# Optimization experiments

Hardware: AMD Instinct MI355X
Metric: run time of the kernel (lower is better)

Reference implementation:

```python
import jax, jax.numpy as jnp
import numpy as np

N = 25000
E = 400000
MUL0 = 64   # multiplicity of 0e node irreps
MUL1 = 32   # multiplicity of 1o node irreps
NUM_BASIS = 10
FC_HIDDEN = 100
WEIGHT_NUMEL = 2 * MUL0 + 3 * MUL1  # 224: per-edge tp weights for the 5 uvu paths
MID_S = MUL0 + MUL1       # 96 mid scalar channels
MID_V = MUL0 + 2 * MUL1   # 128 mid vector channels
NUM_NEIGHBORS = 16.0


def setup_inputs() -> dict:
    key = jax.random.key(0)
    ks = jax.random.split(key, 16)
    inp = {
        'node_scalars': jax.random.normal(ks[0], (N, MUL0), jnp.float32),
        'node_vectors': jax.random.normal(ks[1], (N, MUL1, 3), jnp.float32),
        'node_attr': jnp.ones((N, 1), jnp.float32),
        'edge_src': jax.random.randint(ks[2], (E,), 0, N, jnp.int32),
        'edge_dst': jax.random.randint(ks[3], (E,), 0, N, jnp.int32),
        'edge_attr': jax.random.normal(ks[4], (E, 4), jnp.float32),
        'edge_scalars': jax.random.normal(ks[5], (E, NUM_BASIS), jnp.float32),
        # FullyConnectedNet: [10, 100, weight_numel], silu on hidden
        'W_fc1': jax.random.normal(ks[6], (NUM_BASIS, FC_HIDDEN), jnp.float32) / np.sqrt(NUM_BASIS),
        'W_fc2': jax.random.normal(ks[7], (FC_HIDDEN, WEIGHT_NUMEL), jnp.float32) / np.sqrt(FC_HIDDEN),
        # FullyConnectedTensorProduct with 0e attr == per-irrep linear mixing
        'W_sc_s': jax.random.normal(ks[8], (MUL0, MUL0), jnp.float32) / np.sqrt(MUL0),
        'W_sc_v': jax.random.normal(ks[9], (MUL1, MUL1), jnp.float32) / np.sqrt(MUL1),
        'W_l1_s': jax.random.normal(ks[10], (MUL0, MUL0), jnp.float32) / np.sqrt(MUL0),
        'W_l1_v': jax.random.normal(ks[11], (MUL1, MUL1), jnp.float32) / np.sqrt(MUL1),
        'W_l2_s': jax.random.normal(ks[12], (MID_S, MUL0), jnp.float32) / np.sqrt(MID_S),
        'W_l2_v': jax.random.normal(ks[13], (MID_V, MUL1), jnp.float32) / np.sqrt(MID_V),
        'W_l3': jax.random.normal(ks[14], (MID_S, 1), jnp.float32) / np.sqrt(MID_S),
    }
    return inp


def reference(node_scalars, node_vectors, node_attr, edge_src, edge_dst, edge_attr,
              edge_scalars, W_fc1, W_fc2, W_sc_s, W_sc_v, W_l1_s, W_l1_v,
              W_l2_s, W_l2_v, W_l3):
    n = node_scalars.shape[0]
    # --- edge-weight FC net: silu hidden, linear out -> per-edge tp weights ---
    w = jax.nn.silu(edge_scalars @ W_fc1) @ W_fc2  # [E, 224]
    w_00, w_01 = w[:, :MUL0], w[:, MUL0:2 * MUL0]                  # paths from 0e input
    w_10 = w[:, 2 * MUL0:2 * MUL0 + MUL1]                          # 1o x 0e -> 1o
    w_11s = w[:, 2 * MUL0 + MUL1:2 * MUL0 + 2 * MUL1]              # 1o x 1o -> 0e
    w_11v = w[:, 2 * MUL0 + 2 * MUL1:]                             # 1o x 1o -> 1o

    attr = node_attr  # [N,1] (0e attr => scalar multiplier)
    # self-connection and lin1 (per-irrep linear * attr)
    sc_s = (node_scalars @ W_sc_s) * attr
    sc_v = jnp.einsum('nuc,uv->nvc', node_vectors, W_sc_v) * attr[:, :, None]
    f_s = (node_scalars @ W_l1_s) * attr
    f_v = jnp.einsum('nuc,uv->nvc', node_vectors, W_l1_v) * attr[:, :, None]

    # --- gather source node features per edge ---
    s = f_s[edge_src]          # [E, MUL0]
    v = f_v[edge_src]          # [E, MUL1, 3]
    y0 = edge_attr[:, :1]      # l=0 sh
    y1 = edge_attr[:, 1:4]     # l=1 sh

    # --- weighted tensor product (uvu), CG-contracted paths ---
    mid_s = jnp.concatenate([
        w_00 * s * y0,                                              # 0e x 0e -> 0e
        w_11s * jnp.einsum('euc,ec->eu', v, y1) / jnp.sqrt(3.0),    # 1o x 1o -> 0e
    ], axis=1)                                                      # [E, 96]
    mid_v = jnp.concatenate([
        w_01[:, :, None] * s[:, :, None] * y1[:, None, :],          # 0e x 1o -> 1o
        w_10[:, :, None] * v * y0[:, :, None],                      # 1o x 0e -> 1o
        w_11v[:, :, None] * jnp.cross(v, y1[:, None, :]) / jnp.sqrt(2.0),  # 1o x 1o -> 1o
    ], axis=1)                                                      # [E, 128, 3]

    # --- scatter-add aggregation into destination nodes ---
    inv = 1.0 / jnp.sqrt(NUM_NEIGHBORS)
    agg_s = jax.ops.segment_sum(mid_s, edge_dst, num_segments=n) * inv
    agg_v = jax.ops.segment_sum(mid_v, edge_dst, num_segments=n) * inv

    # --- output linears and gated residual mix ---
    conv_s = (agg_s @ W_l2_s) * attr
    conv_v = jnp.einsum('nuc,uv->nvc', agg_v, W_l2_v) * attr[:, :, None]
    angle = 0.1 * (agg_s @ W_l3) * attr  # [N,1]
    cos, sin = jnp.cos(angle), jnp.sin(angle)  # sc output_mask is all-ones here
    out_s = cos * sc_s + sin * conv_s
    out_v = cos[:, :, None] * sc_v + sin[:, :, None] * conv_v
    return jnp.concatenate([out_s, out_v.reshape(n, -1)], axis=1)  # [N, 64+96]
```

## Files before the change

### kernel.cpp

```cpp
#include <hip/hip_runtime.h>

#define MUL0 64
#define MUL1 32
#define NBASIS 10
#define FCH 100
#define WNUMEL 224
#define MIDS 96
#define MIDV 128
#define EG 4

#define OFF_W1   0
#define OFF_W2   1000
#define OFF_WSCS 23400
#define OFF_WSCV 27496
#define OFF_WL1S 28520
#define OFF_WL1V 32616
#define OFF_WL2S 33640
#define OFF_WL2V 39784
#define OFF_WL3  43880
#define OFF_WEND 43976
#define OFF_FLAG 43980
#define OFF_W1FRAG 44032
#define OFF_W2FRAG 45824
#define OFF_DYN  60160

#define W1FRAG_N (112 * 32)
#define W2FRAG_N (4 * 224 * 32)

typedef __attribute__((ext_vector_type(8))) short short8;
typedef __attribute__((ext_vector_type(4))) float f32x4;

__device__ __forceinline__ float bf2f(unsigned short h) {
    unsigned int u = ((unsigned int)h) << 16;
    float f; __builtin_memcpy(&f, &u, 4); return f;
}
__device__ __forceinline__ unsigned short f2bf(float f) {
    unsigned int u; __builtin_memcpy(&u, &f, 4);
    u += 0x7fffu + ((u >> 16) & 1u);
    return (unsigned short)(u >> 16);
}
__device__ __forceinline__ float fast_silu(float x) {
    return x * __builtin_amdgcn_rcpf(1.0f + __expf(-x));
}
template<bool BF>
__device__ __forceinline__ float ldf(const void* p, size_t i) {
    if constexpr (BF) return bf2f(((const unsigned short*)p)[i]);
    else              return ((const float*)p)[i];
}
template<bool BF>
__device__ __forceinline__ void stf(void* p, size_t i, float v) {
    if constexpr (BF) ((unsigned short*)p)[i] = f2bf(v);
    else              ((float*)p)[i] = v;
}
template<bool BF>
__device__ __forceinline__ f32x4 ld4(const void* p, size_t i) {
    if constexpr (BF) {
        ushort4 h = *(const ushort4*)((const unsigned short*)p + i);
        return (f32x4){bf2f(h.x), bf2f(h.y), bf2f(h.z), bf2f(h.w)};
    } else {
        return *(const f32x4*)((const float*)p + i);
    }
}
__device__ __forceinline__ int wave_incl_scan(int v) {
    int lane = threadIdx.x & 63;
    #pragma unroll
    for (int d = 1; d < 64; d <<= 1) {
        int t = __shfl_up(v, d, 64);
        if (lane >= d) v += t;
    }
    return v;
}

template<bool BF>
__device__ __forceinline__ void node_pre_body(
    const void* __restrict__ ns, const void* __restrict__ nv,
    const void* __restrict__ attr,
    const void* __restrict__ Wl1s, const void* __restrict__ Wl1v,
    float* __restrict__ f_s, float* __restrict__ f_v, int i, int Nn)
{
    int stotal = Nn * MUL0;
    if (i < stotal) {
        int n = i >> 6, j = i & 63;
        float a = 0.f;
        #pragma unroll
        for (int u = 0; u < MUL0; u++)
            a = fmaf(ldf<BF>(ns, (size_t)n * MUL0 + u), ldf<BF>(Wl1s, u * MUL0 + j), a);
        f_s[i] = a * ldf<BF>(attr, n);
    } else {
        int m = i - stotal;
        if (m >= Nn * MUL1 * 3) return;
        int n = m / 96; int idx = m - n * 96;
        int vi = idx / 3; int c = idx - vi * 3;
        float a = 0.f;
        #pragma unroll
        for (int u = 0; u < MUL1; u++)
            a = fmaf(ldf<BF>(nv, (size_t)n * 96 + u * 3 + c), ldf<BF>(Wl1v, u * MUL1 + vi), a);
        f_v[m] = a * ldf<BF>(attr, n);
    }
}

__global__ __launch_bounds__(256) void k_prep(
    const void* __restrict__ ns, const void* __restrict__ nv,
    const void* __restrict__ attr,
    const void* __restrict__ a0, const void* __restrict__ a1,
    const void* __restrict__ a2, const void* __restrict__ a3,
    const void* __restrict__ a4, const void* __restrict__ a5,
    const void* __restrict__ a6, const void* __restrict__ a7,
    const void* __restrict__ a8,
    float* __restrict__ wsf,
    unsigned short* __restrict__ w1frag, unsigned short* __restrict__ w2frag,
    int* __restrict__ cnt, int* __restrict__ flag,
    float* __restrict__ f_s, float* __restrict__ f_v, int Nn)
{
    const bool bf = (((const unsigned int*)attr)[0] == 0x3F803F80u);
    int i = blockIdx.x * 256 + threadIdx.x;
    if (i == 0) *flag = bf ? 1 : 0;

    const int npre = Nn * 160;
    if (i < npre) {
        if (bf) node_pre_body<true >(ns, nv, attr, a4, a5, f_s, f_v, i, Nn);
        else    node_pre_body<false>(ns, nv, attr, a4, a5, f_s, f_v, i, Nn);
        return;
    }
    int m = i - npre;
    if (m < OFF_WEND) {
        const void* p; int off = m;
        if      (m < OFF_W2)   { p = a0; }
        else if (m < OFF_WSCS) { p = a1; off = m - OFF_W2; }
        else if (m < OFF_WSCV) { p = a2; off = m - OFF_WSCS; }
        else if (m < OFF_WL1S) { p = a3; off = m - OFF_WSCV; }
        else if (m < OFF_WL1V) { p = a4; off = m - OFF_WL1S; }
        else if (m < OFF_WL2S) { p = a5; off = m - OFF_WL1V; }
        else if (m < OFF_WL2V) { p = a6; off = m - OFF_WL2S; }
        else if (m < OFF_WL3)  { p = a7; off = m - OFF_WL2V; }
        else                   { p = a8; off = m - OFF_WL3; }
        wsf[m] = bf ? ldf<true>(p, off) : ldf<false>(p, off);
        return;
    }
    m -= OFF_WEND;
    if (m < W1FRAG_N) {
        int col = m >> 5, k = m & 31;
        float v = 0.f;
        if (col < FCH && k < NBASIS)
            v = bf ? ldf<true>(a0, k * FCH + col) : ldf<false>(a0, k * FCH + col);
        w1frag[m] = f2bf(v);
        return;
    }
    m -= W1FRAG_N;
    if (m < W2FRAG_N) {
        int q = m / (224 * 32); int r = m - q * 224 * 32;
        int n = r >> 5; int kk = r & 31;
        int k = q * 32 + kk;
        float v = 0.f;
        if (k < FCH)
            v = bf ? ldf<true>(a1, k * WNUMEL + n) : ldf<false>(a1, k * WNUMEL + n);
        w2frag[m] = f2bf(v);
        return;
    }
    m -= W2FRAG_N;
    if (m < Nn) cnt[m] = 0;
}

__global__ __launch_bounds__(256) void k_hist(
    const int* __restrict__ edst, int* __restrict__ cnt, int Ecnt)
{
    int e = blockIdx.x * 256 + threadIdx.x;
    if (e < Ecnt) atomicAdd(&cnt[edst[e]], 1);
}

__global__ __launch_bounds__(256) void k_scan_blk(
    const int* __restrict__ cnt, int* __restrict__ row_part,
    int* __restrict__ blk_sum, int Nn)
{
    __shared__ int ws4[4];
    int tid = threadIdx.x, lane = tid & 63, wid = tid >> 6;
    int i = blockIdx.x * 256 + tid;
    int v = (i < Nn) ? cnt[i] : 0;
    int incl = wave_incl_scan(v);
    if (lane == 63) ws4[wid] = incl;
    __syncthreads();
    int off = 0;
    #pragma unroll
    for (int w2 = 0; w2 < 4; w2++) off += (w2 < wid) ? ws4[w2] : 0;
    if (i < Nn) row_part[i] = off + incl - v;
    if (tid == 0) blk_sum[blockIdx.x] = ws4[0] + ws4[1] + ws4[2] + ws4[3];
}

__global__ __launch_bounds__(256) void k_scan_top(
    const int* __restrict__ blk_sum, int* __restrict__ blk_off,
    int* __restrict__ row_start, int NB, int Nn)
{
    __shared__ int ws4[4];
    int tid = threadIdx.x, lane = tid & 63, wid = tid >> 6;
    int v = (tid < NB) ? blk_sum[tid] : 0;
    int incl = wave_incl_scan(v);
    if (lane == 63) ws4[wid] = incl;
    __syncthreads();
    int off = 0;
    #pragma unroll
    for (int w2 = 0; w2 < 4; w2++) off += (w2 < wid) ? ws4[w2] : 0;
    if (tid < NB) blk_off[tid] = off + incl - v;
    if (tid == 0) row_start[Nn] = ws4[0] + ws4[1] + ws4[2] + ws4[3];
}

__global__ __launch_bounds__(256) void k_rowfix(
    const int* __restrict__ row_part, const int* __restrict__ blk_off,
    int* __restrict__ row_start, int* __restrict__ cur, int Nn)
{
    int i = blockIdx.x * 256 + threadIdx.x;
    if (i < Nn) { row_start[i] = blk_off[i >> 8] + row_part[i]; cur[i] = 0; }
}

__global__ __launch_bounds__(1024) void k_scan1(
    const int* __restrict__ cnt, int* __restrict__ row_start,
    int* __restrict__ cur, int Nn)
{
    __shared__ int wsum[16];
    __shared__ int s_off, s_tot;
    int tid = threadIdx.x, lane = tid & 63, wid = tid >> 6;
    if (tid == 0) s_off = 0;
    __syncthreads();
    for (int base = 0; base < Nn; base += 1024) {
        int i = base + tid;
        int v = (i < Nn) ? cnt[i] : 0;
        int incl = wave_incl_scan(v);
        if (lane == 63) wsum[wid] = incl;
        __syncthreads();
        if (wid == 0) {
            int wv = (lane < 16) ? wsum[lane] : 0;
            int wincl = wave_incl_scan(wv);
            if (lane < 16) wsum[lane] = wincl - wv;
            if (lane == 15) s_tot = wincl;
        }
        __syncthreads();
        int excl = s_off + wsum[wid] + incl - v;
        if (i < Nn) { row_start[i] = excl; cur[i] = 0; }
        __syncthreads();
        if (tid == 0) s_off += s_tot;
        __syncthreads();
    }
    if (threadIdx.x == 0) row_start[Nn] = s_off;
}

__global__ __launch_bounds__(256) void k_place(
    const int* __restrict__ edst, const int* __restrict__ esrc,
    const void* __restrict__ eattr,
    const int* __restrict__ row_start, int* __restrict__ cur,
    int* __restrict__ perm, int* __restrict__ srcs, float* __restrict__ y4,
    int Ecnt, const int* __restrict__ flag, int extras)
{
    int e = blockIdx.x * 256 + threadIdx.x;
    if (e >= Ecnt) return;
    int d = edst[e];
    int pos = row_start[d] + atomicAdd(&cur[d], 1);
    perm[pos] = e;
    if (extras) {
        srcs[pos] = esrc[e];
        float4 yv;
        if (*flag) {
            const unsigned short* ap = (const unsigned short*)eattr + (size_t)e * 4;
            yv = make_float4(bf2f(ap[0]), bf2f(ap[1]), bf2f(ap[2]), bf2f(ap[3]));
        } else {
            const float* ap = (const float*)eattr + (size_t)e * 4;
            yv = make_float4(ap[0], ap[1], ap[2], ap[3]);
        }
        ((float4*)y4)[pos] = yv;
    }
}

#define HFC_STRIDE 136

__global__ __launch_bounds__(256) void k_fc(
    const void* __restrict__ escal, const int* __restrict__ perm,
    const unsigned short* __restrict__ w1frag, const unsigned short* __restrict__ w2frag,
    unsigned short* __restrict__ wbuf, int Ecnt, const int* __restrict__ flag)
{
    __shared__ __align__(16) unsigned short h_lds[64 * HFC_STRIDE];
    const int tid  = threadIdx.x;
    const int lane = tid & 63;
    const int wave = tid >> 6;
    const int nl   = lane & 15;
    const int quad = lane >> 4;
    const int tb   = blockIdx.x * 64;

    for (int i = tid; i < 64 * 16; i += 256) {
        int row = i >> 4;
        h_lds[row * HFC_STRIDE + 112 + (i & 15)] = 0;
    }

    int eidx = tb + 16 * wave + nl;
    if (eidx >= Ecnt) eidx = Ecnt - 1;
    const int e = perm[eidx];
    short8 a = {0, 0, 0, 0, 0, 0, 0, 0};
    if (*flag) {
        const unsigned int* p = (const unsigned int*)((const unsigned short*)escal + (size_t)e * NBASIS);
        if (quad == 0) {
            unsigned int d0 = p[0], d1 = p[1], d2 = p[2], d3 = p[3];
            a = (short8){(short)d0, (short)(d0 >> 16), (short)d1, (short)(d1 >> 16),
                         (short)d2, (short)(d2 >> 16), (short)d3, (short)(d3 >> 16)};
        } else if (quad == 1) {
            unsigned int d4 = p[4];
            a = (short8){(short)d4, (short)(d4 >> 16), 0, 0, 0, 0, 0, 0};
        }
    } else {
        const float* p = (const float*)escal + (size_t)e * NBASIS;
        if (quad == 0) {
            a = (short8){(short)f2bf(p[0]), (short)f2bf(p[1]), (short)f2bf(p[2]), (short)f2bf(p[3]),
                         (short)f2bf(p[4]), (short)f2bf(p[5]), (short)f2bf(p[6]), (short)f2bf(p[7])};
        } else if (quad == 1) {
            a = (short8){(short)f2bf(p[8]), (short)f2bf(p[9]), 0, 0, 0, 0, 0, 0};
        }
    }

    {
        f32x4 hacc[7];
        #pragma unroll
        for (int t = 0; t < 7; t++) {
            short8 b = *(const short8*)&w1frag[(16 * t + nl) * 32 + quad * 8];
            hacc[t] = __builtin_amdgcn_mfma_f32_16x16x32_bf16(
                a, b, (f32x4){0.f, 0.f, 0.f, 0.f}, 0, 0, 0);
        }
        #pragma unroll
        for (int t = 0; t < 7; t++) {
            #pragma unroll
            for (int r = 0; r < 4; r++)
                h_lds[(16 * wave + quad * 4 + r) * HFC_STRIDE + 16 * t + nl] =
                    f2bf(fast_silu(hacc[t][r]));
        }
    }
    __syncthreads();

    #pragma unroll 2
    for (int t = 0; t < 14; t++) {
        f32x4 c = {0.f, 0.f, 0.f, 0.f};
        #pragma unroll
        for (int q = 0; q < 4; q++) {
            short8 av = *(const short8*)&h_lds[(16 * wave + nl) * HFC_STRIDE + q * 32 + quad * 8];
            short8 b = *(const short8*)&w2frag[((q * 224) + 16 * t + nl) * 32 + quad * 8];
            c = __builtin_amdgcn_mfma_f32_16x16x32_bf16(av, b, c, 0, 0, 0);
        }
        #pragma unroll
        for (int r = 0; r < 4; r++)
            wbuf[(size_t)(tb + 16 * wave + quad * 4 + r) * WNUMEL + 16 * t + nl] = f2bf(c[r]);
    }
}

__global__ __launch_bounds__(256) void k_agg(
    const unsigned short* __restrict__ wbuf,
    const int* __restrict__ srcs, const float* __restrict__ y4,
    const int* __restrict__ row_start,
    const float* __restrict__ f_s, const float* __restrict__ f_v,
    const float* __restrict__ Wl3, const void* __restrict__ attr,
    float* __restrict__ agg_s, float* __restrict__ aggv,
    float* __restrict__ cosb, float* __restrict__ sinb,
    int Nn, const int* __restrict__ flag)
{
    const int tid  = threadIdx.x;
    const int lane = tid & 63;
    const int wave = tid >> 6;
    const int node = blockIdx.x * EG + wave;
    if (node >= Nn) return;

    const int lane2 = lane & 31;
    const bool hi = (lane >= 32);

    const int dlo = row_start[node];
    const int dhi = row_start[node + 1];

    float acc0 = 0.f, acc1 = 0.f;
    float accS0 = 0.f, accS1 = 0.f, accS2 = 0.f;
    float accV0 = 0.f, accV1 = 0.f, accV2 = 0.f;

    const float k14 = 0.25f;
    const float k13 = 0.25f * 0.57735026918962576451f;
    const float k12 = 0.25f * 0.70710678118654752440f;

    #pragma unroll 2
    for (int idx = dlo; idx < dhi; idx++) {
        const int srcn = srcs[idx];
        const float4 y = ((const float4*)y4)[idx];
        const float y0 = y.x, y1x = y.y, y1y = y.z, y1z = y.w;
        const unsigned short* wrow = wbuf + (size_t)idx * WNUMEL;
        const float* fsr = f_s + (size_t)srcn * 64;
        const float* fvr = f_v + (size_t)srcn * 96;

        float fs_l = fsr[lane];
        float v0 = fvr[lane2 * 3 + 0];
        float v1 = fvr[lane2 * 3 + 1];
        float v2 = fvr[lane2 * 3 + 2];

        float w00 = bf2f(wrow[lane]);
        float w01 = bf2f(wrow[64 + lane]);
        float wh  = bf2f(wrow[128 + lane]);
        float wx  = bf2f(wrow[160 + lane]);

        acc0 = fmaf(w00 * fs_l, y0 * k14, acc0);

        float dot = v0 * y1x + v1 * y1y + v2 * y1z;
        acc1 = fmaf(wh * dot, k13, acc1);

        float t1 = w01 * fs_l * k14;
        accS0 = fmaf(t1, y1x, accS0);
        accS1 = fmaf(t1, y1y, accS1);
        accS2 = fmaf(t1, y1z, accS2);

        float cx = v1 * y1z - v2 * y1y;
        float cy = v2 * y1x - v0 * y1z;
        float cz = v0 * y1y - v1 * y1x;
        float e0 = hi ? cx : v0;
        float e1 = hi ? cy : v1;
        float e2 = hi ? cz : v2;
        float tv = hi ? (wx * k12) : (wh * (y0 * k14));
        accV0 = fmaf(e0, tv, accV0);
        accV1 = fmaf(e1, tv, accV1);
        accV2 = fmaf(e2, tv, accV2);
    }

    {
        float* as = agg_s + (size_t)node * MIDS;
        float* av = aggv  + (size_t)node * 384;
        as[lane] = acc0;
        if (hi) as[64 + lane2] = acc1;

        av[0 * 128 + lane] = accS0;
        av[1 * 128 + lane] = accS1;
        av[2 * 128 + lane] = accS2;
        const int vrow = hi ? (96 + lane2) : (64 + lane);
        av[0 * 128 + vrow] = accV0;
        av[1 * 128 + vrow] = accV1;
        av[2 * 128 + vrow] = accV2;

        float avv = acc0 * Wl3[lane];
        if (hi) avv = fmaf(acc1, Wl3[64 + lane2], avv);
        #pragma unroll
        for (int d = 1; d < 64; d <<= 1) avv += __shfl_xor(avv, d);
        if (lane == 0) {
            float at = (*flag) ? ldf<true>(attr, node) : ldf<false>(attr, node);
            float aa = 0.1f * avv * at;
            cosb[node] = __cosf(aa);
            sinb[node] = __sinf(aa);
        }
    }
}

#define WT_STRIDE 164

template<bool BF>
__device__ __forceinline__ void final_s_body(
    const float* __restrict__ agg_s, const void* __restrict__ ns,
    const float* __restrict__ cosb, const float* __restrict__ sinb,
    const void* __restrict__ attr, void* __restrict__ out,
    int Nn, const float* Wt, int lane, int nb)
{
    float acc_sc[8], acc_l2[8];
    int nidx[8];
    #pragma unroll
    for (int r = 0; r < 8; r++) {
        acc_sc[r] = 0.f; acc_l2[r] = 0.f;
        int n = nb + r; nidx[r] = (n < Nn) ? n : (Nn - 1);
    }
    #pragma unroll 2
    for (int t = 0; t < 16; t++) {
        f32x4 wv = *(const f32x4*)&Wt[lane * WT_STRIDE + 4 * t];
        #pragma unroll
        for (int r = 0; r < 8; r++) {
            f32x4 x = ld4<BF>(ns, (size_t)nidx[r] * 64 + 4 * t);
            acc_sc[r] = fmaf(x[0], wv[0], acc_sc[r]);
            acc_sc[r] = fmaf(x[1], wv[1], acc_sc[r]);
            acc_sc[r] = fmaf(x[2], wv[2], acc_sc[r]);
            acc_sc[r] = fmaf(x[3], wv[3], acc_sc[r]);
        }
    }
    #pragma unroll 2
    for (int t = 0; t < 24; t++) {
        f32x4 wv = *(const f32x4*)&Wt[lane * WT_STRIDE + 64 + 4 * t];
        #pragma unroll
        for (int r = 0; r < 8; r++) {
            f32x4 x = *(const f32x4*)(agg_s + (size_t)nidx[r] * 96 + 4 * t);
            acc_l2[r] = fmaf(x[0], wv[0], acc_l2[r]);
            acc_l2[r] = fmaf(x[1], wv[1], acc_l2[r]);
            acc_l2[r] = fmaf(x[2], wv[2], acc_l2[r]);
            acc_l2[r] = fmaf(x[3], wv[3], acc_l2[r]);
        }
    }
    #pragma unroll
    for (int r = 0; r < 8; r++) {
        int n = nb + r;
        if (n < Nn) {
            float cv = cosb[n], sv = sinb[n];
            float at = ldf<BF>(attr, n);
            stf<BF>(out, (size_t)n * 160 + lane, at * (cv * acc_sc[r] + sv * acc_l2[r]));
        }
    }
}

__global__ __launch_bounds__(256) void k_final_s(
    const float* __restrict__ agg_s, const void* __restrict__ ns,
    const float* __restrict__ Wscs, const float* __restrict__ Wl2s,
    const float* __restrict__ cosb, const float* __restrict__ sinb,
    const void* __restrict__ attr, void* __restrict__ out,
    int Nn, const int* __restrict__ flag)
{
    __shared__ float Wt[64 * WT_STRIDE];
    const int tid = threadIdx.x;
    for (int i = tid; i < 160 * 64; i += 256) {
        int u = i >> 6, j = i & 63;
        float w = (u < 64) ? Wscs[u * 64 + j] : Wl2s[(u - 64) * 64 + j];
        Wt[j * WT_STRIDE + u] = w;
    }
    __syncthreads();

    const int lane = tid & 63;
    const int wave = __builtin_amdgcn_readfirstlane(tid >> 6);
    const int nb   = (blockIdx.x * 4 + wave) * 8;
    if (nb >= Nn) return;
    if (*flag) final_s_body<true >(agg_s, ns, cosb, sinb, attr, out, Nn, Wt, lane, nb);
    else       final_s_body<false>(agg_s, ns, cosb, sinb, attr, out, Nn, Wt, lane, nb);
}

template<bool BF>
__device__ __forceinline__ void final_v_body(
    const float* __restrict__ aggv, const void* __restrict__ nv,
    const float* __restrict__ cosb, const float* __restrict__ sinb,
    const void* __restrict__ attr, void* __restrict__ out,
    int Nn, const float* Wt, int lane, int ub)
{
    const int vi   = lane & 31;
    const int grp  = lane >> 5;
    const int NU   = 3 * Nn;
    float acc_sc[8], acc_l2[8];
    int gidx[8], nn_[8], cc_[8];
    #pragma unroll
    for (int r = 0; r < 8; r++) {
        acc_sc[r] = 0.f; acc_l2[r] = 0.f;
        int g = ub + grp * 8 + r;
        if (g > NU - 1) g = NU - 1;
        gidx[r] = g;
        nn_[r] = (int)((unsigned)g / 3u);
        cc_[r] = g - 3 * nn_[r];
    }
    #pragma unroll 2
    for (int t = 0; t < 8; t++) {
        f32x4 wv = *(const f32x4*)&Wt[vi * WT_STRIDE + 4 * t];
        #pragma unroll
        for (int r = 0; r < 8; r++) {
            size_t b = (size_t)nn_[r] * 96 + (size_t)(4 * t) * 3 + cc_[r];
            float x0 = ldf<BF>(nv, b);
            float x1 = ldf<BF>(nv, b + 3);
            float x2 = ldf<BF>(nv, b + 6);
            float x3 = ldf<BF>(nv, b + 9);
            acc_sc[r] = fmaf(x0, wv[0], acc_sc[r]);
            acc_sc[r] = fmaf(x1, wv[1], acc_sc[r]);
            acc_sc[r] = fmaf(x2, wv[2], acc_sc[r]);
            acc_sc[r] = fmaf(x3, wv[3], acc_sc[r]);
        }
    }
    #pragma unroll 2
    for (int t = 0; t < 32; t++) {
        f32x4 wv = *(const f32x4*)&Wt[vi * WT_STRIDE + 32 + 4 * t];
        #pragma unroll
        for (int r = 0; r < 8; r++) {
            f32x4 x = *(const f32x4*)(aggv + (size_t)gidx[r] * 128 + 4 * t);
            acc_l2[r] = fmaf(x[0], wv[0], acc_l2[r]);
            acc_l2[r] = fmaf(x[1], wv[1], acc_l2[r]);
            acc_l2[r] = fmaf(x[2], wv[2], acc_l2[r]);
            acc_l2[r] = fmaf(x[3], wv[3], acc_l2[r]);
        }
    }
    #pragma unroll
    for (int r = 0; r < 8; r++) {
        int g = ub + grp * 8 + r;
        if (g < NU) {
            int n = nn_[r], c = cc_[r];
            float cv = cosb[n], sv = sinb[n];
            float at = ldf<BF>(attr, n);
            stf<BF>(out, (size_t)n * 160 + 64 + vi * 3 + c,
                    at * (cv * acc_sc[r] + sv * acc_l2[r]));
        }
    }
}

__global__ __launch_bounds__(256) void k_final_v(
    const float* __restrict__ aggv, const void* __restrict__ nv,
    const float* __restrict__ Wscv, const float* __restrict__ Wl2v,
    const float* __restrict__ cosb, const float* __restrict__ sinb,
    const void* __restrict__ attr, void* __restrict__ out,
    int Nn, const int* __restrict__ flag)
{
    __shared__ float Wt[32 * WT_STRIDE];
    const int tid = threadIdx.x;
    for (int i = tid; i < 160 * 32; i += 256) {
        int u = i >> 5, j = i & 31;
        float w = (u < 32) ? Wscv[u * 32 + j] : Wl2v[(u - 32) * 32 + j];
        Wt[j * WT_STRIDE + u] = w;
    }
    __syncthreads();

    const int lane = tid & 63;
    const int wave = __builtin_amdgcn_readfirstlane(tid >> 6);
    const int ub   = (blockIdx.x * 4 + wave) * 16;
    if (ub >= 3 * Nn) return;
    if (*flag) final_v_body<true >(aggv, nv, cosb, sinb, attr, out, Nn, Wt, lane, ub);
    else       final_v_body<false>(aggv, nv, cosb, sinb, attr, out, Nn, Wt, lane, ub);
}

#define ES_STRIDE 40
#define H_STRIDE 136
#define WL_STRIDE 225

__global__ __launch_bounds__(256) void k_edge_mfma(
    const void* __restrict__ escal, const void* __restrict__ eattr,
    const void* __restrict__ attr,
    const int* __restrict__ esrc,
    const int* __restrict__ row_start, const int* __restrict__ perm,
    const unsigned short* __restrict__ w1frag, const unsigned short* __restrict__ w2frag,
    const float* __restrict__ Wl3,
    const float* __restrict__ f_s, const float* __restrict__ f_v,
    float* __restrict__ agg_s, float* __restrict__ agg_v,
    float* __restrict__ cosb, float* __restrict__ sinb,
    int Nn, const int* __restrict__ flag)
{
    __shared__ __align__(16) unsigned short es_lds[64 * ES_STRIDE];
    __shared__ __align__(16) unsigned short h_lds[64 * H_STRIDE];
    __shared__ __align__(16) unsigned short w_lds[64 * WL_STRIDE];
    __shared__ float y_lds[64][4];
    __shared__ int   src_lds[64];

    const int tid  = threadIdx.x;
    const int lane = tid & 63;
    const int wave = tid >> 6;
    const int nl   = lane & 15;
    const int quad = lane >> 4;
    const int gbase = blockIdx.x * EG;
    const bool isbf = (*flag != 0);

    for (int i = tid; i < 64 * 22; i += 256) {
        int row = i / 22, k = 10 + (i - row * 22);
        es_lds[row * ES_STRIDE + k] = 0;
    }
    for (int i = tid; i < 64 * 16; i += 256) {
        int row = i >> 4, k = 112 + (i & 15);
        h_lds[row * H_STRIDE + k] = 0;
    }

    const int lane2 = lane & 31;
    const int u0 = lane / 3,  c0 = lane - 3 * u0;
    const int pB = 64 + lane;
    const int uB = pB / 3,    cB = pB - 3 * uB;
    const int p2 = 128 + lane;
    const int u2 = p2 / 3,    c2 = p2 - 3 * u2;
    const int pH = 64 + lane2;
    const int uH = pH / 3,    cH = pH - 3 * uH;
    const bool half = (lane < 32);

    const int node = gbase + wave;
    const int dlo = (node < Nn) ? row_start[node] : 0;
    const int dhi = (node < Nn) ? row_start[node + 1] : 0;

    float acc[9];
    #pragma unroll
    for (int s = 0; s < 9; s++) acc[s] = 0.f;

    const int gend    = (gbase + EG < Nn) ? (gbase + EG) : Nn;
    const int e_start = row_start[gbase];
    const int e_end   = row_start[gend];

    for (int tb = e_start; tb < e_end; tb += 64) {
        const int tcnt = (e_end - tb < 64) ? (e_end - tb) : 64;
        __syncthreads();

        {
            int i = tid & 63, part = tid >> 6;
            if (i < tcnt && part < 2) {
                int e = perm[tb + i];
                if (part == 0) {
                    unsigned int* dstp = (unsigned int*)&es_lds[i * ES_STRIDE];
                    if (isbf) {
                        const unsigned int* srcp =
                            (const unsigned int*)((const unsigned short*)escal + (size_t)e * NBASIS);
                        #pragma unroll
                        for (int t2 = 0; t2 < 5; t2++) dstp[t2] = srcp[t2];
                    } else {
                        const float* srcp = (const float*)escal + (size_t)e * NBASIS;
                        #pragma unroll
                        for (int t2 = 0; t2 < 5; t2++) {
                            unsigned int lo = f2bf(srcp[2 * t2]);
                            unsigned int hi = f2bf(srcp[2 * t2 + 1]);
                            dstp[t2] = lo | (hi << 16);
                        }
                    }
                } else {
                    src_lds[i] = esrc[e];
                    if (isbf) {
                        const unsigned short* ap = (const unsigned short*)eattr + (size_t)e * 4;
                        #pragma unroll
                        for (int t2 = 0; t2 < 4; t2++) y_lds[i][t2] = bf2f(ap[t2]);
                    } else {
                        const float* ap = (const float*)eattr + (size_t)e * 4;
                        #pragma unroll
                        for (int t2 = 0; t2 < 4; t2++) y_lds[i][t2] = ap[t2];
                    }
                }
            }
        }
        __syncthreads();

        {
            short8 a = *(const short8*)&es_lds[(16 * wave + nl) * ES_STRIDE + quad * 8];
            f32x4 hacc[7];
            #pragma unroll
            for (int t = 0; t < 7; t++) {
                short8 b = *(const short8*)&w1frag[(16 * t + nl) * 32 + quad * 8];
                hacc[t] = __builtin_amdgcn_mfma_f32_16x16x32_bf16(
                    a, b, (f32x4){0.f, 0.f, 0.f, 0.f}, 0, 0, 0);
            }
            #pragma unroll
            for (int t = 0; t < 7; t++) {
                #pragma unroll
                for (int r = 0; r < 4; r++)
                    h_lds[(16 * wave + quad * 4 + r) * H_STRIDE + 16 * t + nl] =
                        f2bf(fast_silu(hacc[t][r]));
            }
        }
        __syncthreads();

        #pragma unroll 2
        for (int t = 0; t < 14; t++) {
            f32x4 c = {0.f, 0.f, 0.f, 0.f};
            #pragma unroll
            for (int q = 0; q < 4; q++) {
                short8 a = *(const short8*)&h_lds[(16 * wave + nl) * H_STRIDE + q * 32 + quad * 8];
                short8 b = *(const short8*)&w2frag[((q * 224) + 16 * t + nl) * 32 + quad * 8];
                c = __builtin_amdgcn_mfma_f32_16x16x32_bf16(a, b, c, 0, 0, 0);
            }
            #pragma unroll
            for (int r = 0; r < 4; r++)
                w_lds[(16 * wave + quad * 4 + r) * WL_STRIDE + 16 * t + nl] = f2bf(c[r]);
        }
        __syncthreads();

        {
            int lo = dlo > tb ? dlo : tb;
            int hi = dhi < tb + tcnt ? dhi : tb + tcnt;
            for (int idx = lo; idx < hi; idx++) {
                const int i = idx - tb;
                const int srcn = src_lds[i];
                const float y0  = y_lds[i][0];
                const float y1x = y_lds[i][1];
                const float y1y = y_lds[i][2];
                const float y1z = y_lds[i][3];
                const float* fsr = f_s + (size_t)srcn * 64;
                const float* fvr = f_v + (size_t)srcn * 96;
                const unsigned short* wrow = &w_lds[i * WL_STRIDE];

                float fs_l  = fsr[lane];
                float fs_u0 = fsr[u0];
                float fs_uB = fsr[uB];
                float fs_u2 = fsr[u2];
                float fvA0 = fvr[lane2 * 3], fvA1 = fvr[lane2 * 3 + 1], fvA2 = fvr[lane2 * 3 + 2];
                float fvB0 = fvr[u0 * 3],    fvB1 = fvr[u0 * 3 + 1],    fvB2 = fvr[u0 * 3 + 2];
                float fvH0 = fvr[uH * 3],    fvH1 = fvr[uH * 3 + 1],    fvH2 = fvr[uH * 3 + 2];

                float y1c0 = (c0 == 0) ? y1x : (c0 == 1) ? y1y : y1z;
                float y1cB = (cB == 0) ? y1x : (cB == 1) ? y1y : y1z;
                float y1c2 = (c2 == 0) ? y1x : (c2 == 1) ? y1y : y1z;

                float w_s0 = bf2f(wrow[lane]);
                float w_s1 = bf2f(wrow[160 + lane2]);
                float w_s2 = bf2f(wrow[64 + u0]);
                float w_s3 = bf2f(wrow[64 + uB]);
                float w_s4 = bf2f(wrow[64 + u2]);
                float w_s5 = bf2f(wrow[128 + u0]);
                float w_s6 = bf2f(wrow[128 + uH]);
                float w_s7 = bf2f(wrow[192 + u0]);
                float w_s8 = bf2f(wrow[192 + uH]);

                const float k14 = 0.25f;
                const float k13 = 0.25f * 0.57735026918962576451f;
                const float k12 = 0.25f * 0.70710678118654752440f;

                acc[0] = fmaf(w_s0 * fs_l, y0 * k14, acc[0]);
                {
                    float dot = fvA0 * y1x + fvA1 * y1y + fvA2 * y1z;
                    acc[1] = fmaf(w_s1 * dot, k13, acc[1]);
                }
                acc[2] = fmaf(w_s2 * fs_u0, k14 * y1c0, acc[2]);
                acc[3] = fmaf(w_s3 * fs_uB, k14 * y1cB, acc[3]);
                acc[4] = fmaf(w_s4 * fs_u2, k14 * y1c2, acc[4]);
                {
                    float e5 = (c0 == 0) ? fvB0 : (c0 == 1) ? fvB1 : fvB2;
                    float e6 = (cH == 0) ? fvH0 : (cH == 1) ? fvH1 : fvH2;
                    acc[5] = fmaf(w_s5 * e5, k14 * y0, acc[5]);
                    acc[6] = fmaf(w_s6 * e6, k14 * y0, acc[6]);
                }
                {
                    float cr7 = (c0 == 0) ? (fvB1 * y1z - fvB2 * y1y)
                              : (c0 == 1) ? (fvB2 * y1x - fvB0 * y1z)
                                          : (fvB0 * y1y - fvB1 * y1x);
                    float cr8 = (cH == 0) ? (fvH1 * y1z - fvH2 * y1y)
                              : (cH == 1) ? (fvH2 * y1x - fvH0 * y1z)
                                          : (fvH0 * y1y - fvH1 * y1x);
                    acc[7] = fmaf(w_s7 * cr7, k12, acc[7]);
                    acc[8] = fmaf(w_s8 * cr8, k12, acc[8]);
                }
            }
        }
    }

    if (node < Nn) {
        float* as = agg_s + (size_t)node * MIDS;
        float* av = agg_v + (size_t)node * (MIDV * 3);
        as[lane] = acc[0];
        if (half) as[64 + lane] = acc[1];
        av[lane]       = acc[2];
        av[64 + lane]  = acc[3];
        av[128 + lane] = acc[4];
        av[192 + lane] = acc[5];
        if (half) av[256 + lane] = acc[6];
        av[288 + lane] = acc[7];
        if (half) av[352 + lane] = acc[8];

        float avv = acc[0] * Wl3[lane];
        if (half) avv = fmaf(acc[1], Wl3[64 + lane], avv);
        #pragma unroll
        for (int d = 1; d < 64; d <<= 1) avv += __shfl_xor(avv, d);
        if (lane == 0) {
            float at = isbf ? ldf<true>(attr, node) : ldf<false>(attr, node);
            float a = 0.1f * avv * at;
            cosb[node] = __cosf(a);
            sinb[node] = __sinf(a);
        }
    }
}

template<bool BF>
__device__ __forceinline__ void final_body(
    const void* __restrict__ ns, const void* __restrict__ nv,
    const void* __restrict__ attr,
    const float* __restrict__ Wscs, const float* __restrict__ Wscv,
    const float* __restrict__ Wl2s, const float* __restrict__ Wl2v,
    const float* __restrict__ agg_s, const float* __restrict__ agg_v,
    const float* __restrict__ cosb, const float* __restrict__ sinb,
    void* __restrict__ out, int Nn)
{
    int i = blockIdx.x * 256 + threadIdx.x;
    int stotal = Nn * MUL0;
    if (i < stotal) {
        int n = i >> 6, j = i & 63;
        const float* ar = agg_s + (size_t)n * MIDS;
        float a1 = 0.f, a2 = 0.f;
        #pragma unroll
        for (int u = 0; u < MUL0; u++)
            a1 = fmaf(ldf<BF>(ns, (size_t)n * MUL0 + u), Wscs[u * MUL0 + j], a1);
        #pragma unroll
        for (int u = 0; u < MIDS; u++) a2 = fmaf(ar[u], Wl2s[u * MUL0 + j], a2);
        float o = ldf<BF>(attr, n) * (cosb[n] * a1 + sinb[n] * a2);
        stf<BF>(out, (size_t)n * 160 + j, o);
    } else {
        int m = i - stotal;
        if (m >= Nn * 96) return;
        int n = m / 96; int idx = m - n * 96;
        int vi = idx / 3; int c = idx - vi * 3;
        const float* ar = agg_v + (size_t)n * (MIDV * 3);
        float a1 = 0.f, a2 = 0.f;
        #pragma unroll
        for (int u = 0; u < MUL1; u++)
            a1 = fmaf(ldf<BF>(nv, (size_t)n * 96 + u * 3 + c), Wscv[u * MUL1 + vi], a1);
        #pragma unroll
        for (int u = 0; u < MIDV; u++) a2 = fmaf(ar[u * 3 + c], Wl2v[u * MUL1 + vi], a2);
        float o = ldf<BF>(attr, n) * (cosb[n] * a1 + sinb[n] * a2);
        stf<BF>(out, (size_t)n * 160 + 64 + idx, o);
    }
}
__global__ __launch_bounds__(256) void k_final(
    const void* ns, const void* nv, const void* attr,
    const float* Wscs, const float* Wscv,
    const float* Wl2s, const float* Wl2v,
    const float* agg_s, const float* agg_v,
    const float* cosb, const float* sinb,
    void* out, int Nn, const int* flag)
{
    if (*flag) final_body<true >(ns, nv, attr, Wscs, Wscv, Wl2s, Wl2v, agg_s, agg_v, cosb, sinb, out, Nn);
    else       final_body<false>(ns, nv, attr, Wscs, Wscv, Wl2s, Wl2v, agg_s, agg_v, cosb, sinb, out, Nn);
}

extern "C" void kernel_launch(void* const* d_in, const int* in_sizes, int n_in,
                              void* d_out, int out_size, void* d_ws, size_t ws_size,
                              hipStream_t stream)
{
    const void* ns    = d_in[0];
    const void* nv    = d_in[1];
    const void* attr  = d_in[2];
    const int*  esrc  = (const int*)d_in[3];
    const int*  edst  = (const int*)d_in[4];
    const void* eattr = d_in[5];
    const void* escal = d_in[6];

    const int Nn   = in_sizes[2];
    const int Ecnt = in_sizes[3];

    float* ws = (float*)d_ws;
    int* flag = (int*)(ws + OFF_FLAG);
    unsigned short* w1frag = (unsigned short*)(ws + OFF_W1FRAG);
    unsigned short* w2frag = (unsigned short*)(ws + OFF_W2FRAG);

    size_t o = OFF_DYN;
    const size_t OFF_FS   = o; o += (size_t)Nn * 64;
    const size_t OFF_FV   = o; o += (size_t)Nn * 96;
    const size_t OFF_AGGS = o; o += (size_t)Nn * 96;
    const size_t OFF_AGGV = o; o += (size_t)Nn * 384;
    const size_t OFF_COS  = o; o += Nn;
    const size_t OFF_SIN  = o; o += Nn;
    const size_t OFF_CNT  = o; o += Nn;
    const size_t OFF_ROW  = o; o += Nn + 1;
    const size_t OFF_CUR  = o; o += Nn;
    const size_t OFF_RPART= o; o += Nn;
    const size_t OFF_BSUM = o; o += 256;
    const size_t OFF_BOFF = o; o += 256;
    const size_t OFF_PERM = o; o += Ecnt;
    const size_t OFF_SRCS = o; o += Ecnt;
    o = (o + 3) & ~(size_t)3;
    const size_t OFF_Y4   = o; o += (size_t)Ecnt * 4;
    o = (o + 15) & ~(size_t)15;
    const size_t OFF_WBUF = o;
    const int tiles = (Ecnt + 63) / 64;
    o += (size_t)tiles * 64 * 112;
    const size_t need_bytes = o * sizeof(float);

    int* cnt       = (int*)(ws + OFF_CNT);
    int* row_start = (int*)(ws + OFF_ROW);
    int* cur       = (int*)(ws + OFF_CUR);
    int* row_part  = (int*)(ws + OFF_RPART);
    int* blk_sum   = (int*)(ws + OFF_BSUM);
    int* blk_off   = (int*)(ws + OFF_BOFF);
    int* perm      = (int*)(ws + OFF_PERM);
    int* srcs      = (int*)(ws + OFF_SRCS);
    float* y4      = ws + OFF_Y4;
    unsigned short* wbuf = (unsigned short*)(ws + OFF_WBUF);

    const int NB = (Nn + 255) / 256;
    const bool split = (ws_size >= need_bytes) && (NB <= 256);

    const int prep_work = Nn * 160 + OFF_WEND + W1FRAG_N + W2FRAG_N + Nn;
    k_prep<<<(prep_work + 255) / 256, 256, 0, stream>>>(
        ns, nv, attr,
        d_in[7], d_in[8], d_in[9], d_in[10], d_in[11], d_in[12],
        d_in[13], d_in[14], d_in[15],
        ws, w1frag, w2frag, cnt, flag,
        ws + OFF_FS, ws + OFF_FV, Nn);

    k_hist<<<(Ecnt + 255) / 256, 256, 0, stream>>>(edst, cnt, Ecnt);

    if (split) {
        k_scan_blk<<<NB, 256, 0, stream>>>(cnt, row_part, blk_sum, Nn);
        k_scan_top<<<1, 256, 0, stream>>>(blk_sum, blk_off, row_start, NB, Nn);
        k_rowfix<<<NB, 256, 0, stream>>>(row_part, blk_off, row_start, cur, Nn);
        k_place<<<(Ecnt + 255) / 256, 256, 0, stream>>>(
            edst, esrc, eattr, row_start, cur, perm, srcs, y4, Ecnt, flag, 1);

        k_fc<<<tiles, 256, 0, stream>>>(escal, perm, w1frag, w2frag, wbuf, Ecnt, flag);

        k_agg<<<(Nn + EG - 1) / EG, 256, 0, stream>>>(
            wbuf, srcs, y4, row_start,
            ws + OFF_FS, ws + OFF_FV, ws + OFF_WL3, attr,
            ws + OFF_AGGS, ws + OFF_AGGV, ws + OFF_COS, ws + OFF_SIN,
            Nn, flag);

        k_final_s<<<(Nn + 31) / 32, 256, 0, stream>>>(
            ws + OFF_AGGS, ns, ws + OFF_WSCS, ws + OFF_WL2S,
            ws + OFF_COS, ws + OFF_SIN, attr, (void*)d_out, Nn, flag);
        k_final_v<<<(3 * Nn + 63) / 64, 256, 0, stream>>>(
            ws + OFF_AGGV, nv, ws + OFF_WSCV, ws + OFF_WL2V,
            ws + OFF_COS, ws + OFF_SIN, attr, (void*)d_out, Nn, flag);
    } else {
        k_scan1<<<1, 1024, 0, stream>>>(cnt, row_start, cur, Nn);
        k_place<<<(Ecnt + 255) / 256, 256, 0, stream>>>(
            edst, esrc, eattr, row_start, cur, perm, srcs, y4, Ecnt, flag, 0);
        k_edge_mfma<<<(Nn + EG - 1) / EG, 256, 0, stream>>>(
            escal, eattr, attr, esrc, row_start, perm, w1frag, w2frag,
            ws + OFF_WL3,
            ws + OFF_FS, ws + OFF_FV,
            ws + OFF_AGGS, ws + OFF_AGGV, ws + OFF_COS, ws + OFF_SIN,
            Nn, flag);
        k_final<<<((Nn * 160) + 255) / 256, 256, 0, stream>>>(
            ns, nv, attr,
            ws + OFF_WSCS, ws + OFF_WSCV, ws + OFF_WL2S, ws + OFF_WL2V,
            ws + OFF_AGGS, ws + OFF_AGGV, ws + OFF_COS, ws + OFF_SIN,
            (void*)d_out, Nn, flag);
    }
}
```

Measured before the change: 544.7 us.

## Split node pre-linear into register-tiled kernels, reuse FC2 weights, unroll aggregation edges

The per-node linear layers move out of the prep kernel into two dedicated kernels. Each stages the transposed weight in shared memory and gives every lane several nodes, so each weight load is reused across them. The FC second layer now loads each B fragment once per output tile and reuses it across all four edge groups, with wave tiles split unevenly. The aggregation loop splits each node's edges into four interleaved chains with masked padding, giving more memory-level parallelism at the cost of extra registers and wasted loads on low-degree nodes.

```diff
diff --git a/kernel.cpp b/kernel.cpp
--- a/kernel.cpp
+++ b/kernel.cpp
@@ -71,36 +71,7 @@
     return v;
 }
 
-template<bool BF>
-__device__ __forceinline__ void node_pre_body(
-    const void* __restrict__ ns, const void* __restrict__ nv,
-    const void* __restrict__ attr,
-    const void* __restrict__ Wl1s, const void* __restrict__ Wl1v,
-    float* __restrict__ f_s, float* __restrict__ f_v, int i, int Nn)
-{
-    int stotal = Nn * MUL0;
-    if (i < stotal) {
-        int n = i >> 6, j = i & 63;
-        float a = 0.f;
-        #pragma unroll
-        for (int u = 0; u < MUL0; u++)
-            a = fmaf(ldf<BF>(ns, (size_t)n * MUL0 + u), ldf<BF>(Wl1s, u * MUL0 + j), a);
-        f_s[i] = a * ldf<BF>(attr, n);
-    } else {
-        int m = i - stotal;
-        if (m >= Nn * MUL1 * 3) return;
-        int n = m / 96; int idx = m - n * 96;
-        int vi = idx / 3; int c = idx - vi * 3;
-        float a = 0.f;
-        #pragma unroll
-        for (int u = 0; u < MUL1; u++)
-            a = fmaf(ldf<BF>(nv, (size_t)n * 96 + u * 3 + c), ldf<BF>(Wl1v, u * MUL1 + vi), a);
-        f_v[m] = a * ldf<BF>(attr, n);
-    }
-}
-
 __global__ __launch_bounds__(256) void k_prep(
-    const void* __restrict__ ns, const void* __restrict__ nv,
     const void* __restrict__ attr,
     const void* __restrict__ a0, const void* __restrict__ a1,
     const void* __restrict__ a2, const void* __restrict__ a3,
@@ -109,20 +80,12 @@
     const void* __restrict__ a8,
     float* __restrict__ wsf,
     unsigned short* __restrict__ w1frag, unsigned short* __restrict__ w2frag,
-    int* __restrict__ cnt, int* __restrict__ flag,
-    float* __restrict__ f_s, float* __restrict__ f_v, int Nn)
+    int* __restrict__ cnt, int* __restrict__ flag, int Nn)
 {
     const bool bf = (((const unsigned int*)attr)[0] == 0x3F803F80u);
-    int i = blockIdx.x * 256 + threadIdx.x;
-    if (i == 0) *flag = bf ? 1 : 0;
-
-    const int npre = Nn * 160;
-    if (i < npre) {
-        if (bf) node_pre_body<true >(ns, nv, attr, a4, a5, f_s, f_v, i, Nn);
-        else    node_pre_body<false>(ns, nv, attr, a4, a5, f_s, f_v, i, Nn);
-        return;
-    }
-    int m = i - npre;
+    int m = blockIdx.x * 256 + threadIdx.x;
+    if (m == 0) *flag = bf ? 1 : 0;
+
     if (m < OFF_WEND) {
         const void* p; int off = m;
         if      (m < OFF_W2)   { p = a0; }
@@ -159,6 +122,126 @@
     }
     m -= W2FRAG_N;
     if (m < Nn) cnt[m] = 0;
+}
+
+#define PS_STRIDE 68
+#define PV_STRIDE 36
+
+template<bool BF>
+__device__ __forceinline__ void pre_s_body(
+    const void* __restrict__ ns, const void* __restrict__ attr,
+    const float* Wt, float* __restrict__ f_s, int Nn, int lane, int nb)
+{
+    float acc[8]; int nidx[8];
+    #pragma unroll
+    for (int r = 0; r < 8; r++) {
+        acc[r] = 0.f;
+        int n = nb + r; nidx[r] = (n < Nn) ? n : (Nn - 1);
+    }
+    #pragma unroll 2
+    for (int t = 0; t < 16; t++) {
+        f32x4 wv = *(const f32x4*)&Wt[lane * PS_STRIDE + 4 * t];
+        #pragma unroll
+        for (int r = 0; r < 8; r++) {
+            f32x4 x = ld4<BF>(ns, (size_t)nidx[r] * 64 + 4 * t);
+            acc[r] = fmaf(x[0], wv[0], acc[r]);
+            acc[r] = fmaf(x[1], wv[1], acc[r]);
+            acc[r] = fmaf(x[2], wv[2], acc[r]);
+            acc[r] = fmaf(x[3], wv[3], acc[r]);
+        }
+    }
+    #pragma unroll
+    for (int r = 0; r < 8; r++) {
+        int n = nb + r;
+        if (n < Nn) {
+            float at = ldf<BF>(attr, n);
+            f_s[(size_t)n * 64 + lane] = acc[r] * at;
+        }
+    }
+}
+
+__global__ __launch_bounds__(256) void k_pre_s(
+    const void* __restrict__ ns, const void* __restrict__ attr,
+    const float* __restrict__ Wl1s, float* __restrict__ f_s, int Nn)
+{
+    __shared__ float Wt[64 * PS_STRIDE];
+    const int tid = threadIdx.x;
+    const bool bf = (((const unsigned int*)attr)[0] == 0x3F803F80u);
+    for (int i = tid; i < 64 * 64; i += 256) {
+        int u = i >> 6, j = i & 63;
+        Wt[j * PS_STRIDE + u] = Wl1s[u * 64 + j];
+    }
+    __syncthreads();
+    const int lane = tid & 63;
+    const int wave = __builtin_amdgcn_readfirstlane(tid >> 6);
+    const int nb   = (blockIdx.x * 4 + wave) * 8;
+    if (nb >= Nn) return;
+    if (bf) pre_s_body<true >(ns, attr, Wt, f_s, Nn, lane, nb);
+    else    pre_s_body<false>(ns, attr, Wt, f_s, Nn, lane, nb);
+}
+
+template<bool BF>
+__device__ __forceinline__ void pre_v_body(
+    const void* __restrict__ nv, const void* __restrict__ attr,
+    const float* Wt, float* __restrict__ f_v, int Nn, int lane, int ub)
+{
+    const int vi  = lane & 31;
+    const int grp = lane >> 5;
+    const int NU  = 3 * Nn;
+    float acc[8]; int nn_[8], cc_[8];
+    #pragma unroll
+    for (int r = 0; r < 8; r++) {
+        acc[r] = 0.f;
+        int g = ub + grp * 8 + r;
+        if (g > NU - 1) g = NU - 1;
+        nn_[r] = (int)((unsigned)g / 3u);
+        cc_[r] = g - 3 * nn_[r];
+    }
+    #pragma unroll 2
+    for (int t = 0; t < 8; t++) {
+        f32x4 wv = *(const f32x4*)&Wt[vi * PV_STRIDE + 4 * t];
+        #pragma unroll
+        for (int r = 0; r < 8; r++) {
+            size_t b = (size_t)nn_[r] * 96 + (size_t)(4 * t) * 3 + cc_[r];
+            float x0 = ldf<BF>(nv, b);
+            float x1 = ldf<BF>(nv, b + 3);
+            float x2 = ldf<BF>(nv, b + 6);
+            float x3 = ldf<BF>(nv, b + 9);
+            acc[r] = fmaf(x0, wv[0], acc[r]);
+            acc[r] = fmaf(x1, wv[1], acc[r]);
+            acc[r] = fmaf(x2, wv[2], acc[r]);
+            acc[r] = fmaf(x3, wv[3], acc[r]);
+        }
+    }
+    #pragma unroll
+    for (int r = 0; r < 8; r++) {
+        int g = ub + grp * 8 + r;
+        if (g < NU) {
+            int n = nn_[r], c = cc_[r];
+            float at = ldf<BF>(attr, n);
+            f_v[(size_t)n * 96 + vi * 3 + c] = acc[r] * at;
+        }
+    }
+}
+
+__global__ __launch_bounds__(256) void k_pre_v(
+    const void* __restrict__ nv, const void* __restrict__ attr,
+    const float* __restrict__ Wl1v, float* __restrict__ f_v, int Nn)
+{
+    __shared__ float Wt[32 * PV_STRIDE];
+    const int tid = threadIdx.x;
+    const bool bf = (((const unsigned int*)attr)[0] == 0x3F803F80u);
+    for (int i = tid; i < 32 * 32; i += 256) {
+        int u = i >> 5, vi = i & 31;
+        Wt[vi * PV_STRIDE + u] = Wl1v[u * 32 + vi];
+    }
+    __syncthreads();
+    const int lane = tid & 63;
+    const int wave = __builtin_amdgcn_readfirstlane(tid >> 6);
+    const int ub   = (blockIdx.x * 4 + wave) * 16;
+    if (ub >= 3 * Nn) return;
+    if (bf) pre_v_body<true >(nv, attr, Wt, f_v, Nn, lane, ub);
+    else    pre_v_body<false>(nv, attr, Wt, f_v, Nn, lane, ub);
 }
 
 __global__ __launch_bounds__(256) void k_hist(
@@ -330,18 +413,32 @@
     }
     __syncthreads();
 
-    #pragma unroll 2
-    for (int t = 0; t < 14; t++) {
-        f32x4 c = {0.f, 0.f, 0.f, 0.f};
-        #pragma unroll
-        for (int q = 0; q < 4; q++) {
-            short8 av = *(const short8*)&h_lds[(16 * wave + nl) * HFC_STRIDE + q * 32 + quad * 8];
-            short8 b = *(const short8*)&w2frag[((q * 224) + 16 * t + nl) * 32 + quad * 8];
-            c = __builtin_amdgcn_mfma_f32_16x16x32_bf16(av, b, c, 0, 0, 0);
-        }
-        #pragma unroll
-        for (int r = 0; r < 4; r++)
-            wbuf[(size_t)(tb + 16 * wave + quad * 4 + r) * WNUMEL + 16 * t + nl] = f2bf(c[r]);
+    {
+        const int tsta = (wave < 2) ? wave * 4 : 8 + (wave - 2) * 3;
+        const int tend = (wave < 2) ? tsta + 4 : tsta + 3;
+        for (int t = tsta; t < tend; t++) {
+            short8 b0 = *(const short8*)&w2frag[(0 * 224 + 16 * t + nl) * 32 + quad * 8];
+            short8 b1 = *(const short8*)&w2frag[(1 * 224 + 16 * t + nl) * 32 + quad * 8];
+            short8 b2 = *(const short8*)&w2frag[(2 * 224 + 16 * t + nl) * 32 + quad * 8];
+            short8 b3 = *(const short8*)&w2frag[(3 * 224 + 16 * t + nl) * 32 + quad * 8];
+            #pragma unroll
+            for (int eg = 0; eg < 4; eg++) {
+                const unsigned short* hrow = &h_lds[(16 * eg + nl) * HFC_STRIDE];
+                f32x4 c = {0.f, 0.f, 0.f, 0.f};
+                c = __builtin_amdgcn_mfma_f32_16x16x32_bf16(
+                    *(const short8*)&hrow[0 * 32 + quad * 8], b0, c, 0, 0, 0);
+                c = __builtin_amdgcn_mfma_f32_16x16x32_bf16(
+                    *(const short8*)&hrow[1 * 32 + quad * 8], b1, c, 0, 0, 0);
+                c = __builtin_amdgcn_mfma_f32_16x16x32_bf16(
+                    *(const short8*)&hrow[2 * 32 + quad * 8], b2, c, 0, 0, 0);
+                c = __builtin_amdgcn_mfma_f32_16x16x32_bf16(
+                    *(const short8*)&hrow[3 * 32 + quad * 8], b3, c, 0, 0, 0);
+                #pragma unroll
+                for (int r = 0; r < 4; r++)
+                    wbuf[(size_t)(tb + 16 * eg + quad * 4 + r) * WNUMEL + 16 * t + nl] =
+                        f2bf(c[r]);
+            }
+        }
     }
 }
 
@@ -366,55 +463,68 @@
 
     const int dlo = row_start[node];
     const int dhi = row_start[node + 1];
-
-    float acc0 = 0.f, acc1 = 0.f;
-    float accS0 = 0.f, accS1 = 0.f, accS2 = 0.f;
-    float accV0 = 0.f, accV1 = 0.f, accV2 = 0.f;
+    const int deg = dhi - dlo;
+    const int q   = (deg + 3) >> 2;
 
     const float k14 = 0.25f;
     const float k13 = 0.25f * 0.57735026918962576451f;
     const float k12 = 0.25f * 0.70710678118654752440f;
 
-    #pragma unroll 2
-    for (int idx = dlo; idx < dhi; idx++) {
-        const int srcn = srcs[idx];
-        const float4 y = ((const float4*)y4)[idx];
-        const float y0 = y.x, y1x = y.y, y1y = y.z, y1z = y.w;
-        const unsigned short* wrow = wbuf + (size_t)idx * WNUMEL;
-        const float* fsr = f_s + (size_t)srcn * 64;
-        const float* fvr = f_v + (size_t)srcn * 96;
-
-        float fs_l = fsr[lane];
-        float v0 = fvr[lane2 * 3 + 0];
-        float v1 = fvr[lane2 * 3 + 1];
-        float v2 = fvr[lane2 * 3 + 2];
-
-        float w00 = bf2f(wrow[lane]);
-        float w01 = bf2f(wrow[64 + lane]);
-        float wh  = bf2f(wrow[128 + lane]);
-        float wx  = bf2f(wrow[160 + lane]);
-
-        acc0 = fmaf(w00 * fs_l, y0 * k14, acc0);
-
-        float dot = v0 * y1x + v1 * y1y + v2 * y1z;
-        acc1 = fmaf(wh * dot, k13, acc1);
-
-        float t1 = w01 * fs_l * k14;
-        accS0 = fmaf(t1, y1x, accS0);
-        accS1 = fmaf(t1, y1y, accS1);
-        accS2 = fmaf(t1, y1z, accS2);
-
-        float cx = v1 * y1z - v2 * y1y;
-        float cy = v2 * y1x - v0 * y1z;
-        float cz = v0 * y1y - v1 * y1x;
-        float e0 = hi ? cx : v0;
-        float e1 = hi ? cy : v1;
-        float e2 = hi ? cz : v2;
-        float tv = hi ? (wx * k12) : (wh * (y0 * k14));
-        accV0 = fmaf(e0, tv, accV0);
-        accV1 = fmaf(e1, tv, accV1);
-        accV2 = fmaf(e2, tv, accV2);
-    }
+    float A0[4], A1[4], S0[4], S1[4], S2[4], V0[4], V1[4], V2[4];
+    #pragma unroll
+    for (int c = 0; c < 4; c++) {
+        A0[c] = A1[c] = S0[c] = S1[c] = S2[c] = V0[c] = V1[c] = V2[c] = 0.f;
+    }
+
+    for (int j = 0; j < q; j++) {
+        #pragma unroll
+        for (int c = 0; c < 4; c++) {
+            const int idxr = dlo + c * q + j;
+            const int idx_ = (idxr < dhi) ? idxr : (dhi - 1);
+            const float vm = (idxr < dhi) ? 1.f : 0.f;
+            const int srcn = srcs[idx_];
+            const float4 y = ((const float4*)y4)[idx_];
+            const float y0 = y.x * vm, y1x = y.y * vm, y1y = y.z * vm, y1z = y.w * vm;
+            const unsigned short* wrow = wbuf + (size_t)idx_ * WNUMEL;
+            const float* fsr = f_s + (size_t)srcn * 64;
+            const float* fvr = f_v + (size_t)srcn * 96;
+            float fs_l = fsr[lane];
+            float v0 = fvr[lane2 * 3 + 0];
+            float v1 = fvr[lane2 * 3 + 1];
+            float v2 = fvr[lane2 * 3 + 2];
+            float w00 = bf2f(wrow[lane]);
+            float w01 = bf2f(wrow[64 + lane]);
+            float wh  = bf2f(wrow[128 + lane]);
+            float wx  = bf2f(wrow[160 + lane]);
+
+            A0[c] = fmaf(w00 * fs_l, y0 * k14, A0[c]);
+            float dot_ = v0 * y1x + v1 * y1y + v2 * y1z;
+            A1[c] = fmaf(wh * dot_, k13, A1[c]);
+            float t1_ = w01 * fs_l * k14;
+            S0[c] = fmaf(t1_, y1x, S0[c]);
+            S1[c] = fmaf(t1_, y1y, S1[c]);
+            S2[c] = fmaf(t1_, y1z, S2[c]);
+            float cx_ = v1 * y1z - v2 * y1y;
+            float cy_ = v2 * y1x - v0 * y1z;
+            float cz_ = v0 * y1y - v1 * y1x;
+            float e0_ = hi ? cx_ : v0;
+            float e1_ = hi ? cy_ : v1;
+            float e2_ = hi ? cz_ : v2;
+            float tv_ = hi ? (wx * k12) : (wh * (y0 * k14));
+            V0[c] = fmaf(e0_, tv_, V0[c]);
+            V1[c] = fmaf(e1_, tv_, V1[c]);
+            V2[c] = fmaf(e2_, tv_, V2[c]);
+        }
+    }
+
+    const float acc0  = (A0[0] + A0[1]) + (A0[2] + A0[3]);
+    const float acc1  = (A1[0] + A1[1]) + (A1[2] + A1[3]);
+    const float accS0 = (S0[0] + S0[1]) + (S0[2] + S0[3]);
+    const float accS1 = (S1[0] + S1[1]) + (S1[2] + S1[3]);
+    const float accS2 = (S2[0] + S2[1]) + (S2[2] + S2[3]);
+    const float accV0 = (V0[0] + V0[1]) + (V0[2] + V0[3]);
+    const float accV1 = (V1[0] + V1[1]) + (V1[2] + V1[3]);
+    const float accV2 = (V2[0] + V2[1]) + (V2[2] + V2[3]);
 
     {
         float* as = agg_s + (size_t)node * MIDS;
@@ -941,13 +1051,17 @@
     const int NB = (Nn + 255) / 256;
     const bool split = (ws_size >= need_bytes) && (NB <= 256);
 
-    const int prep_work = Nn * 160 + OFF_WEND + W1FRAG_N + W2FRAG_N + Nn;
+    const int prep_work = OFF_WEND + W1FRAG_N + W2FRAG_N + Nn;
     k_prep<<<(prep_work + 255) / 256, 256, 0, stream>>>(
-        ns, nv, attr,
+        attr,
         d_in[7], d_in[8], d_in[9], d_in[10], d_in[11], d_in[12],
         d_in[13], d_in[14], d_in[15],
-        ws, w1frag, w2frag, cnt, flag,
-        ws + OFF_FS, ws + OFF_FV, Nn);
+        ws, w1frag, w2frag, cnt, flag, Nn);
+
+    k_pre_s<<<(Nn + 31) / 32, 256, 0, stream>>>(
+        ns, attr, ws + OFF_WL1S, ws + OFF_FS, Nn);
+    k_pre_v<<<(3 * Nn + 63) / 64, 256, 0, stream>>>(
+        nv, attr, ws + OFF_WL1V, ws + OFF_FV, Nn);
 
     k_hist<<<(Ecnt + 255) / 256, 256, 0, stream>>>(edst, cnt, Ecnt);
 
```

Result: faster. 486.3 us (-10.7%).
